# Kernel optimization log

Measured on AMD Instinct MI355X. Metric: run time of the kernel, lower is better.

## Reference

```python
import jax, jax.numpy as jnp
import numpy as np

N_NODES = 250000
N_EDGES = 4000000
N_GRAPHS = 512
NEG_SLOPE = 0.01  # F.leaky_relu default


def _glorot(key, shape):
    fan_in, fan_out = shape
    lim = (6.0 / (fan_in + fan_out)) ** 0.5
    return jax.random.uniform(key, shape, jnp.float32, -lim, lim)


def setup_inputs() -> dict:
    key = jax.random.key(0)
    ks = jax.random.split(key, 12)
    x = jax.random.normal(ks[0], (N_NODES, 13), jnp.float32)
    edge_index = jax.random.randint(ks[1], (2, N_EDGES), 0, N_NODES, jnp.int64)
    batch_index = jnp.sort(jax.random.randint(ks[2], (N_NODES,), 0, N_GRAPHS, jnp.int64))
    # SAGEConv params: lin_l (neighbor agg, with bias), lin_r (self, no bias)
    dims = [(13, 16), (16, 8), (8, 4)]
    params = {}
    for i, (di, do) in enumerate(dims, 1):
        params[f'W{i}l'] = _glorot(ks[2 + 2 * i], (di, do))
        params[f'b{i}'] = jnp.zeros((do,), jnp.float32)
        params[f'W{i}r'] = _glorot(ks[3 + 2 * i], (di, do))
    params['Wc'] = _glorot(ks[10], (8, 1))
    params['bc'] = jnp.zeros((1,), jnp.float32)
    return dict(x=x, edge_index=edge_index, batch_index=batch_index, **params)


def _sage_conv(x, src, dst, Wl, bl, Wr):
    # mean-aggregate neighbor features at target nodes, then linear
    msg_sum = jax.ops.segment_sum(x[src], dst, num_segments=N_NODES)  # [N, d]
    cnt = jax.ops.segment_sum(jnp.ones((src.shape[0],), x.dtype), dst,
                              num_segments=N_NODES)
    agg = msg_sum / jnp.maximum(cnt, 1.0)[:, None]
    return agg @ Wl + bl + x @ Wr


def reference(x, edge_index, batch_index,
              W1l, b1, W1r, W2l, b2, W2r, W3l, b3, W3r, Wc, bc):
    src, dst = edge_index[0], edge_index[1]
    h = jax.nn.leaky_relu(_sage_conv(x, src, dst, W1l, b1, W1r), NEG_SLOPE)
    h = jax.nn.leaky_relu(_sage_conv(h, src, dst, W2l, b2, W2r), NEG_SLOPE)
    h = _sage_conv(h, src, dst, W3l, b3, W3r)  # [N, 4]
    add_pool = jax.ops.segment_sum(h, batch_index, num_segments=N_GRAPHS)  # [G,4]
    gcnt = jax.ops.segment_sum(jnp.ones((N_NODES,), h.dtype), batch_index,
                               num_segments=N_GRAPHS)
    mean_pool = add_pool / jnp.maximum(gcnt, 1.0)[:, None]
    g = jnp.concatenate([mean_pool, add_pool], axis=1)  # [G, 8]
    return g @ Wc + bc  # [G, 1]
```

## Files before the change

### kernel.cpp

```cpp
#include <hip/hip_runtime.h>

#define N_NODES 250000
#define N_EDGES 4000000
#define N_GRAPHS 512
#define NEG 0.01f
#define BINB 9
#define WIN 512
#define NBINS 489
#define NSUB (NBINS * 4)
#define CAPQ 2560
#define PART_EPB 8192
#define PART_BLOCKS 489

__device__ __forceinline__ float lrelu(float v) { return v > 0.0f ? v : NEG * v; }
__device__ __forceinline__ unsigned f2b(float f) {
    unsigned u = __float_as_uint(f);
    unsigned r = ((u >> 16) & 1u) + 0x7FFFu;
    return (u + r) >> 16;
}
__device__ __forceinline__ unsigned pk(float a, float b) { return f2b(a) | (f2b(b) << 16); }
__device__ __forceinline__ float blo(unsigned p) { return __uint_as_float(p << 16); }
__device__ __forceinline__ float bhi(unsigned p) { return __uint_as_float(p & 0xFFFF0000u); }

__global__ __launch_bounds__(256) void pack_x(const float* __restrict__ x,
                                              unsigned* __restrict__ x16b,
                                              int* __restrict__ qcnt) {
    if (blockIdx.x == 0) {
        for (int i = threadIdx.x; i < NSUB; i += 256) qcnt[i] = 0;
    }
    int tid = blockIdx.x * blockDim.x + threadIdx.x;
    if (tid >= N_NODES * 8) return;
    int n = tid >> 3, d2 = tid & 7;
    int a = d2 * 2, b = a + 1;
    float va = (a < 13) ? x[n * 13 + a] : 0.0f;
    float vb = (b < 13) ? x[n * 13 + b] : 0.0f;
    x16b[tid] = pk(va, vb);
}

__global__ __launch_bounds__(1024) void partition_k(const int* __restrict__ src,
                                                    const int* __restrict__ dst,
                                                    int* __restrict__ qcnt,
                                                    unsigned* __restrict__ binned) {
    __shared__ int hist[NSUB];
    __shared__ int loff[NSUB];
    __shared__ int base[NSUB];
    __shared__ unsigned ebuf[PART_EPB];
    __shared__ unsigned short subid[PART_EPB];
    __shared__ int wsum[16];
    int t = threadIdx.x;
    for (int i = t; i < NSUB; i += 1024) hist[i] = 0;
    __syncthreads();
    unsigned e0 = blockIdx.x * PART_EPB;
    int m = min((int)PART_EPB, (int)(N_EDGES - e0));
    for (int i = t; i < m; i += 1024) {
        unsigned e = e0 + i;
        int s = ((dst[e] >> BINB) << 2) | (src[e] >> 16);
        atomicAdd(&hist[s], 1);
    }
    __syncthreads();
    int p = 0, s0 = 0, incl = 0;
    if (t < NSUB / 2) { s0 = hist[2 * t]; p = s0 + hist[2 * t + 1]; }
    incl = p;
#pragma unroll
    for (int d = 1; d < 64; d <<= 1) {
        int u = __shfl_up(incl, d, 64);
        if ((t & 63) >= d) incl += u;
    }
    if ((t & 63) == 63) wsum[t >> 6] = incl;
    __syncthreads();
    if (t == 0) {
        int r = 0;
#pragma unroll
        for (int i = 0; i < 16; i++) { int s = wsum[i]; wsum[i] = r; r += s; }
    }
    __syncthreads();
    if (t < NSUB / 2) {
        int ex = incl + wsum[t >> 6] - p;
        loff[2 * t] = ex;
        loff[2 * t + 1] = ex + s0;
    }
    __syncthreads();
    for (int i = t; i < NSUB; i += 1024) {
        int h = hist[i];
        base[i] = (h > 0) ? atomicAdd(&qcnt[i], h) : 0;
    }
    __syncthreads();
    for (int i = t; i < NSUB; i += 1024) hist[i] = loff[i];
    __syncthreads();
    for (int i = t; i < m; i += 1024) {
        unsigned e = e0 + i;
        int d = dst[e], sv = src[e];
        int s = ((d >> BINB) << 2) | (sv >> 16);
        int pos = atomicAdd(&hist[s], 1);
        ebuf[pos] = ((unsigned)(d & (WIN - 1)) << 18) | (unsigned)sv;
        subid[pos] = (unsigned short)s;
    }
    __syncthreads();
    for (int j = t; j < m; j += 1024) {
        int s = subid[j];
        binned[(size_t)s * CAPQ + base[s] + (j - loff[s])] = ebuf[j];
    }
}

__global__ __launch_bounds__(1024) void sortagg_k(const unsigned* __restrict__ x16b,
                                                  unsigned* __restrict__ binned,
                                                  const int* __restrict__ qcnt,
                                                  int* __restrict__ offs,
                                                  float* __restrict__ cntf,
                                                  float* __restrict__ agg) {
    __shared__ unsigned stg[CAPQ];
    __shared__ unsigned srt[CAPQ];
    __shared__ int hist[WIN];
    __shared__ int cur[WIN];
    __shared__ int wsum[8];
    int t = threadIdx.x;
    int bin = blockIdx.x;
    int f = t & (WIN - 1), l = t >> 9;
    int lane = t & 63, wv = t >> 6;
    float a0 = 0, a1 = 0, a2 = 0, a3 = 0, a4 = 0, a5 = 0, a6 = 0, a7 = 0;
    int deg = 0;
    for (int q = 0; q < 4; q++) {
        int sub = (bin << 2) | q;
        int cnt = qcnt[sub];
        unsigned* bp = binned + (size_t)sub * CAPQ;
        if (t < WIN) hist[t] = 0;
        __syncthreads();
        for (int i = t; i < cnt; i += 1024) {
            unsigned w = bp[i];
            stg[i] = w;
            atomicAdd(&hist[w >> 18], 1);
        }
        __syncthreads();
        int v = (t < WIN) ? hist[t] : 0;
#pragma unroll
        for (int d = 1; d < 64; d <<= 1) {
            int u = __shfl_up(v, d, 64);
            if (lane >= d) v += u;
        }
        if (t < WIN && lane == 63) wsum[wv] = v;
        __syncthreads();
        if (t == 0) {
            int r = 0;
#pragma unroll
            for (int i = 0; i < 8; i++) { int s = wsum[i]; wsum[i] = r; r += s; }
        }
        __syncthreads();
        if (t < WIN) {
            int incl = v + wsum[wv];
            int ex = incl - hist[t];
            cur[t] = ex;
            offs[(size_t)sub * 513 + t] = ex;
            deg += hist[t];
        }
        if (t == 0) offs[(size_t)sub * 513 + WIN] = cnt;
        __syncthreads();
        for (int i = t; i < cnt; i += 1024) {
            unsigned w = stg[i];
            int pos = atomicAdd(&cur[w >> 18], 1);
            srt[pos] = w;
        }
        __syncthreads();
        for (int i = t; i < cnt; i += 1024) bp[i] = srt[i];
        int e_ = cur[f];
        int s_ = e_ - hist[f];
        int k = s_;
        for (; k + 4 <= e_; k += 4) {
            unsigned w0 = srt[k], w1 = srt[k + 1], w2 = srt[k + 2], w3 = srt[k + 3];
            uint4 v0 = *(const uint4*)&x16b[(size_t)(w0 & 0x3FFFFu) * 8u + (unsigned)(l * 4)];
            uint4 v1 = *(const uint4*)&x16b[(size_t)(w1 & 0x3FFFFu) * 8u + (unsigned)(l * 4)];
            uint4 v2 = *(const uint4*)&x16b[(size_t)(w2 & 0x3FFFFu) * 8u + (unsigned)(l * 4)];
            uint4 v3 = *(const uint4*)&x16b[(size_t)(w3 & 0x3FFFFu) * 8u + (unsigned)(l * 4)];
            a0 += blo(v0.x) + blo(v1.x) + blo(v2.x) + blo(v3.x);
            a1 += bhi(v0.x) + bhi(v1.x) + bhi(v2.x) + bhi(v3.x);
            a2 += blo(v0.y) + blo(v1.y) + blo(v2.y) + blo(v3.y);
            a3 += bhi(v0.y) + bhi(v1.y) + bhi(v2.y) + bhi(v3.y);
            a4 += blo(v0.z) + blo(v1.z) + blo(v2.z) + blo(v3.z);
            a5 += bhi(v0.z) + bhi(v1.z) + bhi(v2.z) + bhi(v3.z);
            a6 += blo(v0.w) + blo(v1.w) + blo(v2.w) + blo(v3.w);
            a7 += bhi(v0.w) + bhi(v1.w) + bhi(v2.w) + bhi(v3.w);
        }
        for (; k < e_; k++) {
            unsigned w = srt[k];
            uint4 v4 = *(const uint4*)&x16b[(size_t)(w & 0x3FFFFu) * 8u + (unsigned)(l * 4)];
            a0 += blo(v4.x); a1 += bhi(v4.x); a2 += blo(v4.y); a3 += bhi(v4.y);
            a4 += blo(v4.z); a5 += bhi(v4.z); a6 += blo(v4.w); a7 += bhi(v4.w);
        }
        __syncthreads();
    }
    int g = (bin << BINB) + f;
    if (g < N_NODES) {
        size_t b = (size_t)g * 13;
        if (l == 0) {
            agg[b + 0] = a0; agg[b + 1] = a1; agg[b + 2] = a2; agg[b + 3] = a3;
            agg[b + 4] = a4; agg[b + 5] = a5; agg[b + 6] = a6; agg[b + 7] = a7;
            cntf[g] = (float)deg;
        } else {
            agg[b + 8] = a0; agg[b + 9] = a1; agg[b + 10] = a2;
            agg[b + 11] = a3; agg[b + 12] = a4;
        }
    }
}

__global__ __launch_bounds__(256) void fused1(const float* __restrict__ agg,
                                              const float* __restrict__ x,
                                              const float* __restrict__ cntf,
                                              const float* __restrict__ W1l,
                                              const float* __restrict__ b1,
                                              const float* __restrict__ W1r,
                                              const float* __restrict__ W2l,
                                              const float* __restrict__ W2r,
                                              unsigned* __restrict__ y2b,
                                              float* __restrict__ z2) {
    __shared__ float sWl[208], sWr[208], sb[16], sA[128], sB[128];
    for (int i = threadIdx.x; i < 208; i += blockDim.x) { sWl[i] = W1l[i]; sWr[i] = W1r[i]; }
    for (int i = threadIdx.x; i < 128; i += blockDim.x) { sA[i] = W2l[i]; sB[i] = W2r[i]; }
    if (threadIdx.x < 16) sb[threadIdx.x] = b1[threadIdx.x];
    __syncthreads();
    int n = blockIdx.x * blockDim.x + threadIdx.x;
    if (n >= N_NODES) return;
    float inv = 1.0f / fmaxf(cntf[n], 1.0f);
    float a[13], xv[13];
#pragma unroll
    for (int i = 0; i < 13; i++) { a[i] = agg[n * 13 + i] * inv; xv[i] = x[n * 13 + i]; }
    float h[16];
#pragma unroll
    for (int o = 0; o < 16; o++) {
        float acc = sb[o];
#pragma unroll
        for (int i = 0; i < 13; i++) acc += a[i] * sWl[i * 16 + o] + xv[i] * sWr[i * 16 + o];
        h[o] = lrelu(acc);
    }
    float ya[8];
#pragma unroll
    for (int o2 = 0; o2 < 8; o2++) {
        float y = 0.0f, za = 0.0f;
#pragma unroll
        for (int o = 0; o < 16; o++) { y += h[o] * sA[o * 8 + o2]; za += h[o] * sB[o * 8 + o2]; }
        ya[o2] = y;
        z2[n * 8 + o2] = za;
    }
    uint4 out;
    out.x = pk(ya[0], ya[1]); out.y = pk(ya[2], ya[3]);
    out.z = pk(ya[4], ya[5]); out.w = pk(ya[6], ya[7]);
    *(uint4*)&y2b[(size_t)n * 4u] = out;
}

__global__ __launch_bounds__(256) void agg8f_k(const unsigned* __restrict__ y2b,
                                               const unsigned* __restrict__ binned,
                                               const int* __restrict__ offs,
                                               const float* __restrict__ cntf,
                                               const float* __restrict__ b2,
                                               const float* __restrict__ W3l,
                                               float* __restrict__ z2h2,
                                               unsigned* __restrict__ y3b,
                                               float* __restrict__ pool) {
    __shared__ float sb[8], sW3[32];
    if (blockIdx.x == 0) {
        for (int i = threadIdx.x; i < N_GRAPHS * 5; i += 256) pool[i] = 0.0f;
    }
    if (threadIdx.x < 8) sb[threadIdx.x] = b2[threadIdx.x];
    if (threadIdx.x < 32) sW3[threadIdx.x] = W3l[threadIdx.x];
    __syncthreads();
    int g = blockIdx.x * 256 + threadIdx.x;
    if (g >= N_NODES) return;
    int bin = g >> BINB, f = g & (WIN - 1);
    float a0 = 0, a1 = 0, a2 = 0, a3 = 0, a4 = 0, a5 = 0, a6 = 0, a7 = 0;
#pragma unroll
    for (int q = 0; q < 4; q++) {
        int sub = (bin << 2) | q;
        const int* o = offs + (size_t)sub * 513;
        int s = o[f], e = o[f + 1];
        const unsigned* bp = binned + (size_t)sub * CAPQ;
        int k = s;
        for (; k + 4 <= e; k += 4) {
            unsigned w0 = bp[k], w1 = bp[k + 1], w2 = bp[k + 2], w3 = bp[k + 3];
            uint4 v0 = *(const uint4*)&y2b[(size_t)(w0 & 0x3FFFFu) * 4u];
            uint4 v1 = *(const uint4*)&y2b[(size_t)(w1 & 0x3FFFFu) * 4u];
            uint4 v2 = *(const uint4*)&y2b[(size_t)(w2 & 0x3FFFFu) * 4u];
            uint4 v3 = *(const uint4*)&y2b[(size_t)(w3 & 0x3FFFFu) * 4u];
            a0 += blo(v0.x) + blo(v1.x) + blo(v2.x) + blo(v3.x);
            a1 += bhi(v0.x) + bhi(v1.x) + bhi(v2.x) + bhi(v3.x);
            a2 += blo(v0.y) + blo(v1.y) + blo(v2.y) + blo(v3.y);
            a3 += bhi(v0.y) + bhi(v1.y) + bhi(v2.y) + bhi(v3.y);
            a4 += blo(v0.z) + blo(v1.z) + blo(v2.z) + blo(v3.z);
            a5 += bhi(v0.z) + bhi(v1.z) + bhi(v2.z) + bhi(v3.z);
            a6 += blo(v0.w) + blo(v1.w) + blo(v2.w) + blo(v3.w);
            a7 += bhi(v0.w) + bhi(v1.w) + bhi(v2.w) + bhi(v3.w);
        }
        for (; k < e; k++) {
            uint4 v = *(const uint4*)&y2b[(size_t)(bp[k] & 0x3FFFFu) * 4u];
            a0 += blo(v.x); a1 += bhi(v.x); a2 += blo(v.y); a3 += bhi(v.y);
            a4 += blo(v.z); a5 += bhi(v.z); a6 += blo(v.w); a7 += bhi(v.w);
        }
    }
    float inv = 1.0f / fmaxf(cntf[g], 1.0f);
    float h2v[8];
    float s8[8] = {a0, a1, a2, a3, a4, a5, a6, a7};
#pragma unroll
    for (int j = 0; j < 8; j++) {
        float v = s8[j] * inv + sb[j] + z2h2[(size_t)g * 8 + j];
        h2v[j] = lrelu(v);
        z2h2[(size_t)g * 8 + j] = h2v[j];
    }
    float y[4];
#pragma unroll
    for (int k = 0; k < 4; k++) {
        float acc = 0.0f;
#pragma unroll
        for (int j = 0; j < 8; j++) acc += h2v[j] * sW3[j * 4 + k];
        y[k] = acc;
    }
    uint2 out;
    out.x = pk(y[0], y[1]); out.y = pk(y[2], y[3]);
    *(uint2*)&y3b[(size_t)g * 2u] = out;
}

__global__ __launch_bounds__(256) void agg4pool_k(const unsigned* __restrict__ y3b,
                                                  const unsigned* __restrict__ binned,
                                                  const int* __restrict__ offs,
                                                  const float* __restrict__ cntf,
                                                  const float* __restrict__ h2,
                                                  const float* __restrict__ W3r,
                                                  const float* __restrict__ b3,
                                                  const int* __restrict__ batch,
                                                  float* __restrict__ pool,
                                                  float* __restrict__ gcnt) {
    __shared__ float sW[32], sb[4];
    __shared__ float lp[16][4];
    __shared__ float lc[16];
    __shared__ int sbase;
    if (threadIdx.x < 32) sW[threadIdx.x] = W3r[threadIdx.x];
    if (threadIdx.x < 4) sb[threadIdx.x] = b3[threadIdx.x];
    if (threadIdx.x < 16) {
        lc[threadIdx.x] = 0.0f;
        for (int k = 0; k < 4; k++) lp[threadIdx.x][k] = 0.0f;
    }
    int n0 = blockIdx.x * 256;
    if (threadIdx.x == 0) sbase = batch[n0 < N_NODES ? n0 : N_NODES - 1];
    __syncthreads();
    int g = n0 + threadIdx.x;
    if (g < N_NODES) {
        int bin = g >> BINB, f = g & (WIN - 1);
        float a0 = 0, a1 = 0, a2 = 0, a3 = 0;
#pragma unroll
        for (int q = 0; q < 4; q++) {
            int sub = (bin << 2) | q;
            const int* o = offs + (size_t)sub * 513;
            int s = o[f], e = o[f + 1];
            const unsigned* bp = binned + (size_t)sub * CAPQ;
            int k = s;
            for (; k + 4 <= e; k += 4) {
                unsigned w0 = bp[k], w1 = bp[k + 1], w2 = bp[k + 2], w3 = bp[k + 3];
                uint2 v0 = *(const uint2*)&y3b[(size_t)(w0 & 0x3FFFFu) * 2u];
                uint2 v1 = *(const uint2*)&y3b[(size_t)(w1 & 0x3FFFFu) * 2u];
                uint2 v2 = *(const uint2*)&y3b[(size_t)(w2 & 0x3FFFFu) * 2u];
                uint2 v3 = *(const uint2*)&y3b[(size_t)(w3 & 0x3FFFFu) * 2u];
                a0 += blo(v0.x) + blo(v1.x) + blo(v2.x) + blo(v3.x);
                a1 += bhi(v0.x) + bhi(v1.x) + bhi(v2.x) + bhi(v3.x);
                a2 += blo(v0.y) + blo(v1.y) + blo(v2.y) + blo(v3.y);
                a3 += bhi(v0.y) + bhi(v1.y) + bhi(v2.y) + bhi(v3.y);
            }
            for (; k < e; k++) {
                uint2 v = *(const uint2*)&y3b[(size_t)(bp[k] & 0x3FFFFu) * 2u];
                a0 += blo(v.x); a1 += bhi(v.x); a2 += blo(v.y); a3 += bhi(v.y);
            }
        }
        float inv = 1.0f / fmaxf(cntf[g], 1.0f);
        float s4[4] = {a0, a1, a2, a3};
        float h2v[8];
#pragma unroll
        for (int j = 0; j < 8; j++) h2v[j] = h2[(size_t)g * 8 + j];
        int b = batch[g];
        int off = b - sbase;
        bool local = (off >= 0 && off < 16);
#pragma unroll
        for (int k = 0; k < 4; k++) {
            float z = 0.0f;
#pragma unroll
            for (int j = 0; j < 8; j++) z += h2v[j] * sW[j * 4 + k];
            float v = s4[k] * inv + sb[k] + z;
            if (local) atomicAdd(&lp[off][k], v);
            else atomicAdd(&pool[b * 4 + k], v);
        }
        if (local) atomicAdd(&lc[off], 1.0f);
        else atomicAdd(&gcnt[b], 1.0f);
    }
    __syncthreads();
    if (threadIdx.x < 16) {
        int b = sbase + threadIdx.x;
        float c = lc[threadIdx.x];
        if (c > 0.0f && b < N_GRAPHS) {
            atomicAdd(&gcnt[b], c);
            for (int k = 0; k < 4; k++) atomicAdd(&pool[b * 4 + k], lp[threadIdx.x][k]);
        }
    }
}

__global__ __launch_bounds__(256) void final_k(const float* __restrict__ pool,
                                               const float* __restrict__ gcnt,
                                               const float* __restrict__ Wc,
                                               const float* __restrict__ bc,
                                               float* __restrict__ out) {
    int g = blockIdx.x * blockDim.x + threadIdx.x;
    if (g >= N_GRAPHS) return;
    float inv = 1.0f / fmaxf(gcnt[g], 1.0f);
    float acc = bc[0];
#pragma unroll
    for (int k = 0; k < 4; k++) {
        float ap = pool[g * 4 + k];
        acc += ap * inv * Wc[k] + ap * Wc[4 + k];
    }
    out[g] = acc;
}

extern "C" void kernel_launch(void* const* d_in, const int* in_sizes, int n_in,
                              void* d_out, int out_size, void* d_ws, size_t ws_size,
                              hipStream_t stream) {
    const float* x = (const float*)d_in[0];
    const int* ei = (const int*)d_in[1];
    const int* src = ei;
    const int* dst = ei + N_EDGES;
    const int* batch = (const int*)d_in[2];
    const float* W1l = (const float*)d_in[3];
    const float* b1 = (const float*)d_in[4];
    const float* W1r = (const float*)d_in[5];
    const float* W2l = (const float*)d_in[6];
    const float* b2 = (const float*)d_in[7];
    const float* W2r = (const float*)d_in[8];
    const float* W3l = (const float*)d_in[9];
    const float* b3 = (const float*)d_in[10];
    const float* W3r = (const float*)d_in[11];
    const float* Wc = (const float*)d_in[12];
    const float* bc = (const float*)d_in[13];
    float* out = (float*)d_out;

    const size_t N = N_NODES;
    unsigned* binned = (unsigned*)d_ws;
    int* qcnt = (int*)(binned + (size_t)NSUB * CAPQ);
    int* offs = qcnt + 2048;
    float* fbase = (float*)(offs + (size_t)NSUB * 513);
    float* agg = fbase;
    float* cntf = fbase + 13 * N;
    float* z2 = cntf + N;
    unsigned* x16b = (unsigned*)(z2 + 8 * N);
    unsigned* y2b = x16b + 8 * N;
    unsigned* y3b = y2b + 4 * N;
    float* pool = (float*)(y3b + 2 * N);
    float* gcnt = pool + N_GRAPHS * 4;

    const int TPB = 256;
    const int NB = (N_NODES + TPB - 1) / TPB;

    pack_x<<<(N_NODES * 8 + TPB - 1) / TPB, TPB, 0, stream>>>(x, x16b, qcnt);
    partition_k<<<PART_BLOCKS, 1024, 0, stream>>>(src, dst, qcnt, binned);
    sortagg_k<<<NBINS, 1024, 0, stream>>>(x16b, binned, qcnt, offs, cntf, agg);
    fused1<<<NB, TPB, 0, stream>>>(agg, x, cntf, W1l, b1, W1r, W2l, W2r, y2b, z2);
    agg8f_k<<<NB, TPB, 0, stream>>>(y2b, binned, offs, cntf, b2, W3l, z2, y3b, pool);
    agg4pool_k<<<NB, TPB, 0, stream>>>(y3b, binned, offs, cntf, z2, W3r, b3, batch, pool, gcnt);
    final_k<<<2, TPB, 0, stream>>>(pool, gcnt, Wc, bc, out);
}
```

Measured before the change: 269.9 us.

## Sort all four sub-bins concurrently in sortagg instead of serially

The counting sort in sortagg_k now gives each 256-thread group one of the four sub-bins and sorts them at the same time. All four sorted sub-bins stay in shared memory, and the gather-accumulate pass then walks over them. This replaces four serial rounds, each with several block-wide barriers, by a single round. The staging buffer is gone and the binned words are read twice from global memory instead of being staged. Shared memory use rises to about 57 KB, which may lower occupancy.

```diff
diff --git a/kernel.cpp b/kernel.cpp
--- a/kernel.cpp
+++ b/kernel.cpp
@@ -108,64 +108,78 @@
                                                   int* __restrict__ offs,
                                                   float* __restrict__ cntf,
                                                   float* __restrict__ agg) {
-    __shared__ unsigned stg[CAPQ];
-    __shared__ unsigned srt[CAPQ];
-    __shared__ int hist[WIN];
-    __shared__ int cur[WIN];
-    __shared__ int wsum[8];
+    __shared__ unsigned srt[4][CAPQ];
+    __shared__ int hist[4][WIN];
+    __shared__ int cur[4][WIN];
+    __shared__ int wsum[16];
     int t = threadIdx.x;
     int bin = blockIdx.x;
+    int g = t >> 8;
+    int tl = t & 255;
+    int sub = (bin << 2) | g;
+    int cnt = qcnt[sub];
+    unsigned* bp = binned + (size_t)sub * CAPQ;
+    int lane = t & 63, wv = t >> 6;
+
+    for (int i = t; i < 4 * WIN; i += 1024) (&hist[0][0])[i] = 0;
+    __syncthreads();
+
+    for (int i = tl; i < cnt; i += 256) {
+        unsigned w = bp[i];
+        atomicAdd(&hist[g][w >> 18], 1);
+    }
+    __syncthreads();
+
+    int s0 = hist[g][2 * tl];
+    int p = s0 + hist[g][2 * tl + 1];
+    int incl = p;
+#pragma unroll
+    for (int d = 1; d < 64; d <<= 1) {
+        int u = __shfl_up(incl, d, 64);
+        if (lane >= d) incl += u;
+    }
+    if (lane == 63) wsum[wv] = incl;
+    __syncthreads();
+    if (t == 0) {
+#pragma unroll
+        for (int gg = 0; gg < 4; gg++) {
+            int r = 0;
+#pragma unroll
+            for (int i = 0; i < 4; i++) { int s = wsum[gg * 4 + i]; wsum[gg * 4 + i] = r; r += s; }
+        }
+    }
+    __syncthreads();
+    {
+        int ex = incl + wsum[wv] - p;
+        cur[g][2 * tl] = ex;
+        cur[g][2 * tl + 1] = ex + s0;
+        offs[(size_t)sub * 513 + 2 * tl] = ex;
+        offs[(size_t)sub * 513 + 2 * tl + 1] = ex + s0;
+        if (tl == 0) offs[(size_t)sub * 513 + WIN] = cnt;
+    }
+    __syncthreads();
+
+    for (int i = tl; i < cnt; i += 256) {
+        unsigned w = bp[i];
+        int pos = atomicAdd(&cur[g][w >> 18], 1);
+        srt[g][pos] = w;
+    }
+    __syncthreads();
+
+    for (int i = tl; i < cnt; i += 256) bp[i] = srt[g][i];
+
     int f = t & (WIN - 1), l = t >> 9;
-    int lane = t & 63, wv = t >> 6;
     float a0 = 0, a1 = 0, a2 = 0, a3 = 0, a4 = 0, a5 = 0, a6 = 0, a7 = 0;
     int deg = 0;
     for (int q = 0; q < 4; q++) {
-        int sub = (bin << 2) | q;
-        int cnt = qcnt[sub];
-        unsigned* bp = binned + (size_t)sub * CAPQ;
-        if (t < WIN) hist[t] = 0;
-        __syncthreads();
-        for (int i = t; i < cnt; i += 1024) {
-            unsigned w = bp[i];
-            stg[i] = w;
-            atomicAdd(&hist[w >> 18], 1);
-        }
-        __syncthreads();
-        int v = (t < WIN) ? hist[t] : 0;
-#pragma unroll
-        for (int d = 1; d < 64; d <<= 1) {
-            int u = __shfl_up(v, d, 64);
-            if (lane >= d) v += u;
-        }
-        if (t < WIN && lane == 63) wsum[wv] = v;
-        __syncthreads();
-        if (t == 0) {
-            int r = 0;
-#pragma unroll
-            for (int i = 0; i < 8; i++) { int s = wsum[i]; wsum[i] = r; r += s; }
-        }
-        __syncthreads();
-        if (t < WIN) {
-            int incl = v + wsum[wv];
-            int ex = incl - hist[t];
-            cur[t] = ex;
-            offs[(size_t)sub * 513 + t] = ex;
-            deg += hist[t];
-        }
-        if (t == 0) offs[(size_t)sub * 513 + WIN] = cnt;
-        __syncthreads();
-        for (int i = t; i < cnt; i += 1024) {
-            unsigned w = stg[i];
-            int pos = atomicAdd(&cur[w >> 18], 1);
-            srt[pos] = w;
-        }
-        __syncthreads();
-        for (int i = t; i < cnt; i += 1024) bp[i] = srt[i];
-        int e_ = cur[f];
-        int s_ = e_ - hist[f];
+        int e_ = cur[q][f];
+        int h = hist[q][f];
+        int s_ = e_ - h;
+        deg += h;
+        const unsigned* sp = srt[q];
         int k = s_;
         for (; k + 4 <= e_; k += 4) {
-            unsigned w0 = srt[k], w1 = srt[k + 1], w2 = srt[k + 2], w3 = srt[k + 3];
+            unsigned w0 = sp[k], w1 = sp[k + 1], w2 = sp[k + 2], w3 = sp[k + 3];
             uint4 v0 = *(const uint4*)&x16b[(size_t)(w0 & 0x3FFFFu) * 8u + (unsigned)(l * 4)];
             uint4 v1 = *(const uint4*)&x16b[(size_t)(w1 & 0x3FFFFu) * 8u + (unsigned)(l * 4)];
             uint4 v2 = *(const uint4*)&x16b[(size_t)(w2 & 0x3FFFFu) * 8u + (unsigned)(l * 4)];
@@ -180,20 +194,19 @@
             a7 += bhi(v0.w) + bhi(v1.w) + bhi(v2.w) + bhi(v3.w);
         }
         for (; k < e_; k++) {
-            unsigned w = srt[k];
+            unsigned w = sp[k];
             uint4 v4 = *(const uint4*)&x16b[(size_t)(w & 0x3FFFFu) * 8u + (unsigned)(l * 4)];
             a0 += blo(v4.x); a1 += bhi(v4.x); a2 += blo(v4.y); a3 += bhi(v4.y);
             a4 += blo(v4.z); a5 += bhi(v4.z); a6 += blo(v4.w); a7 += bhi(v4.w);
         }
-        __syncthreads();
-    }
-    int g = (bin << BINB) + f;
-    if (g < N_NODES) {
-        size_t b = (size_t)g * 13;
+    }
+    int gn = (bin << BINB) + f;
+    if (gn < N_NODES) {
+        size_t b = (size_t)gn * 13;
         if (l == 0) {
             agg[b + 0] = a0; agg[b + 1] = a1; agg[b + 2] = a2; agg[b + 3] = a3;
             agg[b + 4] = a4; agg[b + 5] = a5; agg[b + 6] = a6; agg[b + 7] = a7;
-            cntf[g] = (float)deg;
+            cntf[gn] = (float)deg;
         } else {
             agg[b + 8] = a0; agg[b + 9] = a1; agg[b + 10] = a2;
             agg[b + 11] = a3; agg[b + 12] = a4;
```

After: 286.1 us. +6.0%, slower.

## Software-pipeline next sub-bin load and histogram in sortagg kernel

Applied to the files above, without the earlier changes.

The sortagg kernel now issues the global loads for the next sub-bin's edge words into registers before sorting and gathering the current one, then builds the next histogram after the gather. A double-buffered histogram removes a separate zeroing barrier and one load/histogram barrier per iteration. The aim is to hide global load latency behind the gather work. It costs extra registers and assumes CAPQ stays at or below 3072 entries, which holds for 2560.

```diff
diff --git a/kernel.cpp b/kernel.cpp
--- a/kernel.cpp
+++ b/kernel.cpp
@@ -110,28 +110,42 @@
                                                   float* __restrict__ agg) {
     __shared__ unsigned stg[CAPQ];
     __shared__ unsigned srt[CAPQ];
-    __shared__ int hist[WIN];
+    __shared__ int histb[2][WIN];
     __shared__ int cur[WIN];
     __shared__ int wsum[8];
     int t = threadIdx.x;
     int bin = blockIdx.x;
     int f = t & (WIN - 1), l = t >> 9;
     int lane = t & 63, wv = t >> 6;
+    int cq[4];
+#pragma unroll
+    for (int q = 0; q < 4; q++) cq[q] = qcnt[(bin << 2) | q];
+
     float a0 = 0, a1 = 0, a2 = 0, a3 = 0, a4 = 0, a5 = 0, a6 = 0, a7 = 0;
     int deg = 0;
+
+    if (t < WIN) histb[0][t] = 0;
+    __syncthreads();
+    {
+        const unsigned* bp0 = binned + (size_t)(bin << 2) * CAPQ;
+        for (int i = t; i < cq[0]; i += 1024) {
+            unsigned w = bp0[i];
+            stg[i] = w;
+            atomicAdd(&histb[0][w >> 18], 1);
+        }
+    }
+    __syncthreads();
+
     for (int q = 0; q < 4; q++) {
+        int cnt = cq[q];
         int sub = (bin << 2) | q;
-        int cnt = qcnt[sub];
+        int* hb = histb[q & 1];
+        int* hn = histb[(q & 1) ^ 1];
         unsigned* bp = binned + (size_t)sub * CAPQ;
-        if (t < WIN) hist[t] = 0;
-        __syncthreads();
-        for (int i = t; i < cnt; i += 1024) {
-            unsigned w = bp[i];
-            stg[i] = w;
-            atomicAdd(&hist[w >> 18], 1);
-        }
-        __syncthreads();
-        int v = (t < WIN) ? hist[t] : 0;
+
+        int v = 0;
+        if (t < WIN) v = hb[t];
+        else hn[t - WIN] = 0;
 #pragma unroll
         for (int d = 1; d < 64; d <<= 1) {
             int u = __shfl_up(v, d, 64);
@@ -147,22 +161,32 @@
         __syncthreads();
         if (t < WIN) {
             int incl = v + wsum[wv];
-            int ex = incl - hist[t];
+            int ex = incl - hb[t];
             cur[t] = ex;
             offs[(size_t)sub * 513 + t] = ex;
-            deg += hist[t];
+            deg += hb[t];
         }
         if (t == 0) offs[(size_t)sub * 513 + WIN] = cnt;
         __syncthreads();
+
+        unsigned sw0 = 0, sw1 = 0, sw2 = 0;
+        int c1 = (q < 3) ? cq[q + 1] : 0;
+        const unsigned* bpn = binned + (size_t)(sub + 1) * CAPQ;
+        if (t < c1) sw0 = bpn[t];
+        if (t + 1024 < c1) sw1 = bpn[t + 1024];
+        if (t + 2048 < c1) sw2 = bpn[t + 2048];
+
         for (int i = t; i < cnt; i += 1024) {
             unsigned w = stg[i];
             int pos = atomicAdd(&cur[w >> 18], 1);
             srt[pos] = w;
         }
         __syncthreads();
+
         for (int i = t; i < cnt; i += 1024) bp[i] = srt[i];
+
         int e_ = cur[f];
-        int s_ = e_ - hist[f];
+        int s_ = e_ - hb[f];
         int k = s_;
         for (; k + 4 <= e_; k += 4) {
             unsigned w0 = srt[k], w1 = srt[k + 1], w2 = srt[k + 2], w3 = srt[k + 3];
@@ -185,15 +209,20 @@
             a0 += blo(v4.x); a1 += bhi(v4.x); a2 += blo(v4.y); a3 += bhi(v4.y);
             a4 += blo(v4.z); a5 += bhi(v4.z); a6 += blo(v4.w); a7 += bhi(v4.w);
         }
+
+        if (t < c1) { stg[t] = sw0; atomicAdd(&hn[sw0 >> 18], 1); }
+        if (t + 1024 < c1) { stg[t + 1024] = sw1; atomicAdd(&hn[sw1 >> 18], 1); }
+        if (t + 2048 < c1) { stg[t + 2048] = sw2; atomicAdd(&hn[sw2 >> 18], 1); }
         __syncthreads();
     }
-    int g = (bin << BINB) + f;
-    if (g < N_NODES) {
-        size_t b = (size_t)g * 13;
+
+    int gn = (bin << BINB) + f;
+    if (gn < N_NODES) {
+        size_t b = (size_t)gn * 13;
         if (l == 0) {
             agg[b + 0] = a0; agg[b + 1] = a1; agg[b + 2] = a2; agg[b + 3] = a3;
             agg[b + 4] = a4; agg[b + 5] = a5; agg[b + 6] = a6; agg[b + 7] = a7;
-            cntf[g] = (float)deg;
+            cntf[gn] = (float)deg;
         } else {
             agg[b + 8] = a0; agg[b + 9] = a1; agg[b + 10] = a2;
             agg[b + 11] = a3; agg[b + 12] = a4;
```

After: 282.1 us. 4.5% more time.

## Fuse layer-1 transform into sort-aggregate kernel and merge packing with partitioning

Applied to the files above, without the earlier changes.

The x packing kernel becomes extra blocks of the partition kernel, and the qcnt reset moves to a memset. The layer-1 linear, leaky ReLU and layer-2 projections now run at the end of the sort-aggregate kernel. Partial sums go through shared memory that reuses the sort buffers, so the 13-float agg array is no longer written and read back through global memory and two launches are removed. In exchange, only half the threads of each 1024-thread block do the dense math, and the union raises that kernel's shared-memory use.

```diff
diff --git a/kernel.cpp b/kernel.cpp
--- a/kernel.cpp
+++ b/kernel.cpp
@@ -11,6 +11,7 @@
 #define CAPQ 2560
 #define PART_EPB 8192
 #define PART_BLOCKS 489
+#define PACK_BLOCKS 1954
 
 __device__ __forceinline__ float lrelu(float v) { return v > 0.0f ? v : NEG * v; }
 __device__ __forceinline__ unsigned f2b(float f) {
@@ -22,25 +23,23 @@
 __device__ __forceinline__ float blo(unsigned p) { return __uint_as_float(p << 16); }
 __device__ __forceinline__ float bhi(unsigned p) { return __uint_as_float(p & 0xFFFF0000u); }
 
-__global__ __launch_bounds__(256) void pack_x(const float* __restrict__ x,
-                                              unsigned* __restrict__ x16b,
-                                              int* __restrict__ qcnt) {
-    if (blockIdx.x == 0) {
-        for (int i = threadIdx.x; i < NSUB; i += 256) qcnt[i] = 0;
-    }
-    int tid = blockIdx.x * blockDim.x + threadIdx.x;
-    if (tid >= N_NODES * 8) return;
-    int n = tid >> 3, d2 = tid & 7;
-    int a = d2 * 2, b = a + 1;
-    float va = (a < 13) ? x[n * 13 + a] : 0.0f;
-    float vb = (b < 13) ? x[n * 13 + b] : 0.0f;
-    x16b[tid] = pk(va, vb);
-}
-
-__global__ __launch_bounds__(1024) void partition_k(const int* __restrict__ src,
+__global__ __launch_bounds__(1024) void part_pack_k(const int* __restrict__ src,
                                                     const int* __restrict__ dst,
                                                     int* __restrict__ qcnt,
-                                                    unsigned* __restrict__ binned) {
+                                                    unsigned* __restrict__ binned,
+                                                    const float* __restrict__ x,
+                                                    unsigned* __restrict__ x16b) {
+    if (blockIdx.x >= PART_BLOCKS) {
+        int tid = (blockIdx.x - PART_BLOCKS) * 1024 + threadIdx.x;
+        if (tid < N_NODES * 8) {
+            int n = tid >> 3, d2 = tid & 7;
+            int a = d2 * 2, b = a + 1;
+            float va = (a < 13) ? x[n * 13 + a] : 0.0f;
+            float vb = (b < 13) ? x[n * 13 + b] : 0.0f;
+            x16b[tid] = pk(va, vb);
+        }
+        return;
+    }
     __shared__ int hist[NSUB];
     __shared__ int loff[NSUB];
     __shared__ int base[NSUB];
@@ -103,20 +102,35 @@
 }
 
 __global__ __launch_bounds__(1024) void sortagg_k(const unsigned* __restrict__ x16b,
+                                                  const float* __restrict__ x,
                                                   unsigned* __restrict__ binned,
                                                   const int* __restrict__ qcnt,
                                                   int* __restrict__ offs,
                                                   float* __restrict__ cntf,
-                                                  float* __restrict__ agg) {
-    __shared__ unsigned stg[CAPQ];
-    __shared__ unsigned srt[CAPQ];
+                                                  const float* __restrict__ W1l,
+                                                  const float* __restrict__ b1,
+                                                  const float* __restrict__ W1r,
+                                                  const float* __restrict__ W2l,
+                                                  const float* __restrict__ W2r,
+                                                  unsigned* __restrict__ y2b,
+                                                  float* __restrict__ z2) {
+    __shared__ union {
+        unsigned sort[2 * CAPQ];
+        float nf[WIN * 13];
+    } u;
     __shared__ int hist[WIN];
     __shared__ int cur[WIN];
     __shared__ int wsum[8];
+    __shared__ float sWl[208], sWr[208], sb1[16], sA[128], sB[128];
+    unsigned* stg = u.sort;
+    unsigned* srt = u.sort + CAPQ;
     int t = threadIdx.x;
     int bin = blockIdx.x;
     int f = t & (WIN - 1), l = t >> 9;
     int lane = t & 63, wv = t >> 6;
+    for (int i = t; i < 208; i += 1024) { sWl[i] = W1l[i]; sWr[i] = W1r[i]; }
+    for (int i = t; i < 128; i += 1024) { sA[i] = W2l[i]; sB[i] = W2r[i]; }
+    if (t < 16) sb1[t] = b1[t];
     float a0 = 0, a1 = 0, a2 = 0, a3 = 0, a4 = 0, a5 = 0, a6 = 0, a7 = 0;
     int deg = 0;
     for (int q = 0; q < 4; q++) {
@@ -134,8 +148,8 @@
         int v = (t < WIN) ? hist[t] : 0;
 #pragma unroll
         for (int d = 1; d < 64; d <<= 1) {
-            int u = __shfl_up(v, d, 64);
-            if (lane >= d) v += u;
+            int uu = __shfl_up(v, d, 64);
+            if (lane >= d) v += uu;
         }
         if (t < WIN && lane == 63) wsum[wv] = v;
         __syncthreads();
@@ -187,62 +201,54 @@
         }
         __syncthreads();
     }
-    int g = (bin << BINB) + f;
-    if (g < N_NODES) {
-        size_t b = (size_t)g * 13;
-        if (l == 0) {
-            agg[b + 0] = a0; agg[b + 1] = a1; agg[b + 2] = a2; agg[b + 3] = a3;
-            agg[b + 4] = a4; agg[b + 5] = a5; agg[b + 6] = a6; agg[b + 7] = a7;
-            cntf[g] = (float)deg;
-        } else {
-            agg[b + 8] = a0; agg[b + 9] = a1; agg[b + 10] = a2;
-            agg[b + 11] = a3; agg[b + 12] = a4;
-        }
-    }
-}
-
-__global__ __launch_bounds__(256) void fused1(const float* __restrict__ agg,
-                                              const float* __restrict__ x,
-                                              const float* __restrict__ cntf,
-                                              const float* __restrict__ W1l,
-                                              const float* __restrict__ b1,
-                                              const float* __restrict__ W1r,
-                                              const float* __restrict__ W2l,
-                                              const float* __restrict__ W2r,
-                                              unsigned* __restrict__ y2b,
-                                              float* __restrict__ z2) {
-    __shared__ float sWl[208], sWr[208], sb[16], sA[128], sB[128];
-    for (int i = threadIdx.x; i < 208; i += blockDim.x) { sWl[i] = W1l[i]; sWr[i] = W1r[i]; }
-    for (int i = threadIdx.x; i < 128; i += blockDim.x) { sA[i] = W2l[i]; sB[i] = W2r[i]; }
-    if (threadIdx.x < 16) sb[threadIdx.x] = b1[threadIdx.x];
-    __syncthreads();
-    int n = blockIdx.x * blockDim.x + threadIdx.x;
-    if (n >= N_NODES) return;
-    float inv = 1.0f / fmaxf(cntf[n], 1.0f);
-    float a[13], xv[13];
-#pragma unroll
-    for (int i = 0; i < 13; i++) { a[i] = agg[n * 13 + i] * inv; xv[i] = x[n * 13 + i]; }
-    float h[16];
-#pragma unroll
-    for (int o = 0; o < 16; o++) {
-        float acc = sb[o];
-#pragma unroll
-        for (int i = 0; i < 13; i++) acc += a[i] * sWl[i * 16 + o] + xv[i] * sWr[i * 16 + o];
-        h[o] = lrelu(acc);
-    }
-    float ya[8];
-#pragma unroll
-    for (int o2 = 0; o2 < 8; o2++) {
-        float y = 0.0f, za = 0.0f;
-#pragma unroll
-        for (int o = 0; o < 16; o++) { y += h[o] * sA[o * 8 + o2]; za += h[o] * sB[o * 8 + o2]; }
-        ya[o2] = y;
-        z2[n * 8 + o2] = za;
-    }
-    uint4 out;
-    out.x = pk(ya[0], ya[1]); out.y = pk(ya[2], ya[3]);
-    out.z = pk(ya[4], ya[5]); out.w = pk(ya[6], ya[7]);
-    *(uint4*)&y2b[(size_t)n * 4u] = out;
+
+    int gn = (bin << BINB) + f;
+    bool act = (l == 0) && (gn < N_NODES);
+    float xr[13];
+    if (act) {
+#pragma unroll
+        for (int i = 0; i < 13; i++) xr[i] = x[(size_t)gn * 13 + i];
+    }
+    if (l == 0) {
+        float* r = &u.nf[f * 13];
+        r[0] = a0; r[1] = a1; r[2] = a2; r[3] = a3;
+        r[4] = a4; r[5] = a5; r[6] = a6; r[7] = a7;
+    } else {
+        float* r = &u.nf[f * 13];
+        r[8] = a0; r[9] = a1; r[10] = a2; r[11] = a3; r[12] = a4;
+    }
+    __syncthreads();
+    if (act) {
+        float dg = (float)deg;
+        cntf[gn] = dg;
+        float inv = 1.0f / fmaxf(dg, 1.0f);
+        float h[16];
+#pragma unroll
+        for (int o = 0; o < 16; o++) h[o] = sb1[o];
+#pragma unroll
+        for (int i = 0; i < 13; i++) {
+            float ai = u.nf[f * 13 + i] * inv;
+            float xi = xr[i];
+#pragma unroll
+            for (int o = 0; o < 16; o++) h[o] += ai * sWl[i * 16 + o] + xi * sWr[i * 16 + o];
+        }
+#pragma unroll
+        for (int o = 0; o < 16; o++) h[o] = lrelu(h[o]);
+        float ya[8], za[8];
+#pragma unroll
+        for (int o2 = 0; o2 < 8; o2++) {
+            float yv = 0.0f, zv = 0.0f;
+#pragma unroll
+            for (int o = 0; o < 16; o++) { yv += h[o] * sA[o * 8 + o2]; zv += h[o] * sB[o * 8 + o2]; }
+            ya[o2] = yv; za[o2] = zv;
+        }
+        *(float4*)&z2[(size_t)gn * 8] = make_float4(za[0], za[1], za[2], za[3]);
+        *(float4*)&z2[(size_t)gn * 8 + 4] = make_float4(za[4], za[5], za[6], za[7]);
+        uint4 outv;
+        outv.x = pk(ya[0], ya[1]); outv.y = pk(ya[2], ya[3]);
+        outv.z = pk(ya[4], ya[5]); outv.w = pk(ya[6], ya[7]);
+        *(uint4*)&y2b[(size_t)gn * 4u] = outv;
+    }
 }
 
 __global__ __launch_bounds__(256) void agg8f_k(const unsigned* __restrict__ y2b,
@@ -447,14 +453,15 @@
     unsigned* y3b = y2b + 4 * N;
     float* pool = (float*)(y3b + 2 * N);
     float* gcnt = pool + N_GRAPHS * 4;
+    (void)agg;
 
     const int TPB = 256;
     const int NB = (N_NODES + TPB - 1) / TPB;
 
-    pack_x<<<(N_NODES * 8 + TPB - 1) / TPB, TPB, 0, stream>>>(x, x16b, qcnt);
-    partition_k<<<PART_BLOCKS, 1024, 0, stream>>>(src, dst, qcnt, binned);
-    sortagg_k<<<NBINS, 1024, 0, stream>>>(x16b, binned, qcnt, offs, cntf, agg);
-    fused1<<<NB, TPB, 0, stream>>>(agg, x, cntf, W1l, b1, W1r, W2l, W2r, y2b, z2);
+    hipMemsetAsync(qcnt, 0, NSUB * sizeof(int), stream);
+    part_pack_k<<<PART_BLOCKS + PACK_BLOCKS, 1024, 0, stream>>>(src, dst, qcnt, binned, x, x16b);
+    sortagg_k<<<NBINS, 1024, 0, stream>>>(x16b, x, binned, qcnt, offs, cntf,
+                                          W1l, b1, W1r, W2l, W2r, y2b, z2);
     agg8f_k<<<NB, TPB, 0, stream>>>(y2b, binned, offs, cntf, b2, W3l, z2, y3b, pool);
     agg4pool_k<<<NB, TPB, 0, stream>>>(y3b, binned, offs, cntf, z2, W3r, b3, batch, pool, gcnt);
     final_k<<<2, TPB, 0, stream>>>(pool, gcnt, Wc, bc, out);
```

New measurement: 307.8 us. 1.14x slower.
